# Performance work log

Hardware: AMD Instinct MI355X
Metric: run time of the kernel (lower is better)

## Reference

```python
import jax, jax.numpy as jnp
import numpy as np

B, N = 16, 2048
EMB_DIM = 512
K = 20          # neighbor_num
S = 1           # support_num

def _norm(x, axis):
    # F.normalize: x / max(||x||, 1e-12)
    return x / jnp.maximum(jnp.linalg.norm(x, axis=axis, keepdims=True), 1e-12)

def knn(verts, k):
    # verts: (b, v, 3); squared-distance knn excluding self
    inner = jnp.einsum('bvd,bwd->bvw', verts, verts)
    quad = jnp.sum(verts * verts, axis=2)
    dist = quad[:, :, None] - 2.0 * inner + quad[:, None, :]
    _, idx = jax.lax.top_k(-dist, k + 1)
    return idx[:, :, 1:]

def gather_nb(x, idx):
    # x: (b, v, c), idx: (b, v, n) -> (b, v, n, c)
    return jax.vmap(lambda t, i: t[i])(x, idx)

def dir_norm(verts, idx):
    d = gather_nb(verts, idx) - verts[:, :, None, :]
    return _norm(d, -1)

def conv_surface(idx, verts, directions, kernel_num):
    theta = jax.nn.relu(jnp.einsum('bvnd,dk->bvnk', dir_norm(verts, idx), _norm(directions, 0)))
    b, v, n, _ = theta.shape
    theta = theta.reshape(b, v, n, S, kernel_num)
    return jnp.sum(jnp.max(theta, axis=2), axis=2)  # (b, v, kernel_num)

def conv_layer(idx, verts, fm, w, bias, directions, out_ch):
    theta = jax.nn.relu(jnp.einsum('bvnd,dk->bvnk', dir_norm(verts, idx), _norm(directions, 0)))
    feat = fm @ w + bias                            # (b, v, (S+1)*out_ch)
    center = feat[:, :, :out_ch]
    support = gather_nb(feat[:, :, out_ch:], idx)   # (b, v, n, S*out_ch)
    b, v, n, _ = support.shape
    act = (theta * support).reshape(b, v, n, S, out_ch)
    return center + jnp.sum(jnp.max(act, axis=2), axis=2)

def pool_layer(verts, fm, key, pooling_rate=4, neighbor_num=4):
    b, v, _ = verts.shape
    idx = knn(verts, neighbor_num)
    pooled = jnp.max(gather_nb(fm, idx), axis=2)
    samp = jax.random.permutation(key, v)[: v // pooling_rate]
    return verts[:, samp, :], pooled[:, samp, :]

def _forward(xyz, w1, b1, w2, b2, w3, b3, w4, b4, fcw, fcb, dir0,
             wc1, bc1, dir1, wc2, bc2, dir2, wc3, bc3, dir3, wc4, bc4, dir4,
             clw1, clb1, bn_gamma, bn_beta, clw2, clb2):
    relu = jax.nn.relu
    # PointNet trunk (Conv1d with kernel 1 == per-point matmul)
    x = relu(jnp.einsum('oc,bcn->bon', w1, xyz) + b1[None, :, None])
    x = relu(jnp.einsum('oc,bcn->bon', w2, x) + b2[None, :, None])
    gf = jnp.max(x, axis=2, keepdims=True)
    x = jnp.concatenate([x, jnp.broadcast_to(gf, x.shape)], axis=1)
    x = relu(jnp.einsum('oc,bcn->bon', w3, x) + b3[None, :, None])
    x = relu(jnp.einsum('oc,bcn->bon', w4, x) + b4[None, :, None])
    x = jnp.max(x, axis=2)                          # (B, 1024)
    # GCN3D trunk
    verts = jnp.transpose(xyz, (0, 2, 1))           # (B, N, 3)
    idx = knn(verts, K)
    fm0 = relu(conv_surface(idx, verts, dir0, 32))
    fm1 = relu(conv_layer(idx, verts, fm0, wc1, bc1, dir1, 64))
    verts, fm1 = pool_layer(verts, fm1, jax.random.key(1))
    idx = knn(verts, K)
    fm2 = relu(conv_layer(idx, verts, fm1, wc2, bc2, dir2, 128))
    fm3 = relu(conv_layer(idx, verts, fm2, wc3, bc3, dir3, 256))
    verts, fm3 = pool_layer(verts, fm3, jax.random.key(2))
    idx = knn(verts, K)
    fm4 = conv_layer(idx, verts, fm3, wc4, bc4, dir4, 1024)
    fg = jnp.max(fm4, axis=1)                       # (B, 1024)
    fc_data = jnp.concatenate([x, fg], axis=1)      # (B, 2048)
    embedding = fc_data @ fcw.T + fcb
    # classifier, eval mode: Dropout -> identity; BN uses running mean 0 / var 1
    h = fc_data @ clw1.T + clb1
    h = relu(h / jnp.sqrt(1.0 + 1e-5) * bn_gamma + bn_beta)
    pred = h @ clw2.T + clb2
    return embedding, pred

def setup_inputs():
    key = jax.random.key(0)
    ks = jax.random.split(key, 32)
    rn = lambda k, shp: jax.random.normal(k, shp, dtype=jnp.float32) * 0.05
    return {
        'xyz': jax.random.normal(ks[0], (B, 3, N), dtype=jnp.float32),
        'w1': rn(ks[1], (64, 3)), 'b1': rn(ks[2], (64,)),
        'w2': rn(ks[3], (128, 64)), 'b2': rn(ks[4], (128,)),
        'w3': rn(ks[5], (256, 256)), 'b3': rn(ks[6], (256,)),
        'w4': rn(ks[7], (1024, 256)), 'b4': rn(ks[8], (1024,)),
        'fcw': rn(ks[9], (EMB_DIM, 2048)), 'fcb': rn(ks[10], (EMB_DIM,)),
        'dir0': rn(ks[11], (3, 32)),
        'wc1': rn(ks[12], (32, 128)), 'bc1': rn(ks[13], (128,)), 'dir1': rn(ks[14], (3, 64)),
        'wc2': rn(ks[15], (64, 256)), 'bc2': rn(ks[16], (256,)), 'dir2': rn(ks[17], (3, 128)),
        'wc3': rn(ks[18], (128, 512)), 'bc3': rn(ks[19], (512,)), 'dir3': rn(ks[20], (3, 256)),
        'wc4': rn(ks[21], (256, 2048)), 'bc4': rn(ks[22], (2048,)), 'dir4': rn(ks[23], (3, 1024)),
        'clw1': rn(ks[24], (512, 2048)), 'clb1': rn(ks[25], (512,)),
        'bn_gamma': jnp.ones((512,), dtype=jnp.float32),
        'bn_beta': jnp.zeros((512,), dtype=jnp.float32),
        'clw2': rn(ks[26], (6, 512)), 'clb2': rn(ks[27], (6,)),
    }

def reference(xyz, w1, b1, w2, b2, w3, b3, w4, b4, fcw, fcb, dir0, wc1, bc1, dir1, wc2, bc2, dir2, wc3, bc3, dir3, wc4, bc4, dir4, clw1, clb1, bn_gamma, bn_beta, clw2, clb2):
    return _forward(xyz, w1, b1, w2, b2, w3, b3, w4, b4, fcw, fcb, dir0, wc1, bc1, dir1, wc2, bc2, dir2, wc3, bc3, dir3, wc4, bc4, dir4, clw1, clb1, bn_gamma, bn_beta, clw2, clb2)
```

## Files before the change

kernel.cpp:

```cpp
#include <hip/hip_runtime.h>
#include <hip/hip_bf16.h>
#include <math.h>

#define BB 16
#define NN 2048

typedef __attribute__((ext_vector_type(8))) short s8v;
typedef __attribute__((ext_vector_type(4))) float f4v;

__global__ void k_sentinel(float* o, int n, float v){
  int i = blockIdx.x*256 + threadIdx.x;
  if (i < n) o[i] = v;
}

__device__ __forceinline__ ushort f2bf(float x){
  unsigned u = __float_as_uint(x);
  unsigned r = u + 0x7FFFu + ((u>>16)&1u);
  return (ushort)(r>>16);
}
__device__ __forceinline__ void splitbf(float v, ushort &h, ushort &l){
  h = f2bf(v);
  float hf = __uint_as_float((unsigned)h<<16);
  l = f2bf(v-hf);
}


__global__ void k_wsplit3h(const float* __restrict__ s1, ushort* __restrict__ d1h, int n1,
                           const float* __restrict__ s2, ushort* __restrict__ d2h, int n2,
                           const float* __restrict__ s3, ushort* __restrict__ d3h, int n3){
  int id = blockIdx.x*256 + threadIdx.x;
  const float* s; ushort *dh; int i;
  if (id < n1){ s=s1; dh=d1h; i=id; }
  else if (id < n1+n2){ s=s2; dh=d2h; i=id-n1; }
  else if (id < n1+n2+n3){ s=s3; dh=d3h; i=id-n1-n2; }
  else return;
  dh[i] = f2bf(s[i]);
}

__global__ void k_wstr4(const float* __restrict__ s1, ushort* __restrict__ d1h, ushort* __restrict__ d1l, int K1, int C1,
                        const float* __restrict__ s2, ushort* __restrict__ d2h, ushort* __restrict__ d2l, int K2, int C2,
                        const float* __restrict__ s3, ushort* __restrict__ d3h, ushort* __restrict__ d3l, int K3, int C3,
                        const float* __restrict__ s4, ushort* __restrict__ d4h, ushort* __restrict__ d4l, int K4, int C4){
  int id = blockIdx.x*256 + threadIdx.x;
  int n1=K1*C1, n2=K2*C2, n3=K3*C3, n4=K4*C4;
  const float* s; ushort *dh, *dl; int i, K, C;
  if (id < n1){ s=s1; dh=d1h; dl=d1l; i=id; K=K1; C=C1; }
  else if (id < n1+n2){ s=s2; dh=d2h; dl=d2l; i=id-n1; K=K2; C=C2; }
  else if (id < n1+n2+n3){ s=s3; dh=d3h; dl=d3l; i=id-n1-n2; K=K3; C=C3; }
  else if (id < n1+n2+n3+n4){ s=s4; dh=d4h; dl=d4l; i=id-n1-n2-n3; K=K4; C=C4; }
  else return;
  int c = i % C, k = i / C;
  ushort h,l; splitbf(s[i], h, l);
  dh[(size_t)c*K + k]=h; dl[(size_t)c*K + k]=l;
}


__global__ void k_mlp1s(const float* __restrict__ xyz, const float* __restrict__ w1,
                        const float* __restrict__ b1, ushort* __restrict__ xh,
                        ushort* __restrict__ xl){
  int id = blockIdx.x*256 + threadIdx.x;
  if (id >= BB*NN*64) return;
  int o = id & 63, n = (id>>6) & (NN-1), b = id>>17;
  float acc = b1[o];
  #pragma unroll
  for (int c=0;c<3;c++)
    acc += w1[o*3+c] * xyz[(size_t)(b*3+c)*NN + n];
  acc = fmaxf(acc, 0.f);
  ushort h,l; splitbf(acc, h, l);
  xh[id]=h; xl[id]=l;
}

__global__ void k_gmax(const float* __restrict__ pmax, ushort* __restrict__ gh,
                       ushort* __restrict__ gl, int parts, int total){
  int id = blockIdx.x*256 + threadIdx.x;
  if (id >= total) return;
  float m = pmax[(size_t)id*parts];
  for (int k=1;k<parts;k++) m = fmaxf(m, pmax[(size_t)id*parts+k]);
  ushort h,l; splitbf(m, h, l);
  gh[id]=h; gl[id]=l;
}

template<int EPI, int RELU, int BCOL>
__global__ __launch_bounds__(256) void k_bgemm(
    const ushort* __restrict__ Ahg,
    const ushort* __restrict__ Bhg, const ushort* __restrict__ Blg,
    const ushort* __restrict__ gfh, const ushort* __restrict__ gfl,
    const float* __restrict__ bias,
    float* __restrict__ outp, float* __restrict__ pmaxp,
    ushort* __restrict__ oth, ushort* __restrict__ otl,
    int K, int ksplit, int Kb, int N, size_t sBT, size_t sOut, int M)
{
  __shared__ ushort Ah[128][40];
  __shared__ ushort Bh[64][40], Bl[64][40];
  __shared__ float red[2][128];
  int t = threadIdx.x, z = blockIdx.z;
  int o0 = blockIdx.y*128, n0 = blockIdx.x*64;
  int wid = t>>6, lane = t&63;
  int wm = wid>>1, wn = wid&1;
  int lr = lane&15, kg = lane>>4;

  f4v acc[4][2];
  #pragma unroll
  for (int i=0;i<4;i++)
    #pragma unroll
    for (int j=0;j<2;j++) acc[i][j] = (f4v){0.f,0.f,0.f,0.f};

  for (int k0=0; k0<K; k0+=32){
    __syncthreads();
    #pragma unroll
    for (int i=0;i<2;i++){
      int j = i*256+t, oo = j>>2, k8 = (j&3)*8;
      size_t sp = (size_t)(o0+oo)*K + k0 + k8;
      *(s8v*)&Ah[oo][k8] = *(const s8v*)(Ahg+sp);
    }
    {
      int nn = t>>2, k8 = (t&3)*8, gk = k0+k8;
      const ushort *sh, *sl;
      if (gk < ksplit){
        size_t sp = (size_t)z*sBT + (size_t)(n0+nn)*Kb + gk;
        sh = Bhg+sp; sl = Blg+sp;
      } else {
        size_t sp = (size_t)z*(K-ksplit) + (gk-ksplit);
        sh = gfh+sp; sl = gfl+sp;
      }
      *(s8v*)&Bh[nn][k8] = *(const s8v*)sh;
      *(s8v*)&Bl[nn][k8] = *(const s8v*)sl;
    }
    __syncthreads();

    s8v ah[4], bh[2], bl[2];
    #pragma unroll
    for (int mt=0;mt<4;mt++){
      int row = wm*64 + mt*16 + lr;
      ah[mt] = *(const s8v*)&Ah[row][kg*8];
    }
    #pragma unroll
    for (int nt=0;nt<2;nt++){
      int col = wn*32 + nt*16 + lr;
      bh[nt] = *(const s8v*)&Bh[col][kg*8];
      bl[nt] = *(const s8v*)&Bl[col][kg*8];
    }
    #pragma unroll
    for (int mt=0;mt<4;mt++)
      #pragma unroll
      for (int nt=0;nt<2;nt++){
        acc[mt][nt] = __builtin_amdgcn_mfma_f32_16x16x32_bf16(ah[mt], bh[nt], acc[mt][nt], 0,0,0);
        acc[mt][nt] = __builtin_amdgcn_mfma_f32_16x16x32_bf16(ah[mt], bl[nt], acc[mt][nt], 0,0,0);
      }
  }

  if (EPI == 1 || EPI == 4){
    #pragma unroll
    for (int mt=0;mt<4;mt++){
      #pragma unroll
      for (int e=0;e<4;e++){
        int row = o0 + wm*64 + mt*16 + kg*4 + e;
        float bv = bias[row];
        float v0 = fmaxf(acc[mt][0][e]+bv, 0.f);
        float v1 = fmaxf(acc[mt][1][e]+bv, 0.f);
        if (EPI == 4){
          int col0 = n0 + wn*32 + lr;
          ushort h,l;
          splitbf(v0, h, l);
          size_t p0 = ((size_t)z*N + col0)*(size_t)M + row;
          oth[p0]=h; otl[p0]=l;
          splitbf(v1, h, l);
          size_t p1 = ((size_t)z*N + col0+16)*(size_t)M + row;
          oth[p1]=h; otl[p1]=l;
        }
        float m = fmaxf(v0, v1);
        m = fmaxf(m, __shfl_xor(m, 1, 64));
        m = fmaxf(m, __shfl_xor(m, 2, 64));
        m = fmaxf(m, __shfl_xor(m, 4, 64));
        m = fmaxf(m, __shfl_xor(m, 8, 64));
        if (lr == 0) red[wn][wm*64 + mt*16 + kg*4 + e] = m;
      }
    }
    __syncthreads();
    if (t < 128){
      float m = fmaxf(red[0][t], red[1][t]);
      pmaxp[((size_t)z*M + o0 + t)*gridDim.x + blockIdx.x] = m;
    }
  } else {
    #pragma unroll
    for (int mt=0;mt<4;mt++){
      #pragma unroll
      for (int nt=0;nt<2;nt++){
        int col = n0 + wn*32 + nt*16 + lr;
        #pragma unroll
        for (int e=0;e<4;e++){
          int row = o0 + wm*64 + mt*16 + kg*4 + e;
          float bv = BCOL ? bias[col] : bias[row];
          float v = acc[mt][nt][e] + bv;
          if (RELU) v = fmaxf(v, 0.f);
          if (EPI == 0)
            outp[(size_t)z*sOut + (size_t)row*N + col] = v;
          if (EPI == 3){
            ushort h,l; splitbf(v, h, l);
            size_t p = ((size_t)z*N + col)*(size_t)M + row;
            oth[p]=h; otl[p]=l;
          }
        }
      }
    }
  }
}

__global__ void k_xmax(const float* __restrict__ pmax, float* __restrict__ xmax){
  int id = blockIdx.x*256 + threadIdx.x;
  if (id >= BB*1024) return;
  float m = pmax[(size_t)id*32];
  for (int k=1;k<32;k++) m = fmaxf(m, pmax[(size_t)id*32+k]);
  xmax[id] = m;
}


#define TF2BODY \
  unsigned ks2 = 0x1BD11BDAu ^ k0 ^ k1; \
  unsigned a = x0 + k0, b = x1 + k1; \
  { \
  a += b; b = (b<<13)|(b>>19); b ^= a; \
  a += b; b = (b<<15)|(b>>17); b ^= a; \
  a += b; b = (b<<26)|(b>>6);  b ^= a; \
  a += b; b = (b<<6) |(b>>26); b ^= a;  a += k1;  b += ks2 + 1u; \
  a += b; b = (b<<17)|(b>>15); b ^= a; \
  a += b; b = (b<<29)|(b>>3);  b ^= a; \
  a += b; b = (b<<16)|(b>>16); b ^= a; \
  a += b; b = (b<<24)|(b>>8);  b ^= a;  a += ks2; b += k0  + 2u; \
  a += b; b = (b<<13)|(b>>19); b ^= a; \
  a += b; b = (b<<15)|(b>>17); b ^= a; \
  a += b; b = (b<<26)|(b>>6);  b ^= a; \
  a += b; b = (b<<6) |(b>>26); b ^= a;  a += k0;  b += k1  + 3u; \
  a += b; b = (b<<17)|(b>>15); b ^= a; \
  a += b; b = (b<<29)|(b>>3);  b ^= a; \
  a += b; b = (b<<16)|(b>>16); b ^= a; \
  a += b; b = (b<<24)|(b>>8);  b ^= a;  a += k1;  b += ks2 + 4u; \
  a += b; b = (b<<13)|(b>>19); b ^= a; \
  a += b; b = (b<<15)|(b>>17); b ^= a; \
  a += b; b = (b<<26)|(b>>6);  b ^= a; \
  a += b; b = (b<<6) |(b>>26); b ^= a;  a += ks2; b += k0  + 5u; \
  } \
  o0 = a; o1 = b;

__device__ __forceinline__ void tf2(unsigned k0, unsigned k1, unsigned x0, unsigned x1,
                                    unsigned &o0, unsigned &o1){ TF2BODY }
static void tf2h(unsigned k0, unsigned k1, unsigned x0, unsigned x1,
                 unsigned &o0, unsigned &o1){ TF2BODY }

__global__ void k_permkeys3(unsigned a0, unsigned a1, unsigned* __restrict__ ka,
                            unsigned b0, unsigned b1, unsigned* __restrict__ kb,
                            unsigned c0, unsigned c1, unsigned* __restrict__ kc){
  int id = blockIdx.x*256 + threadIdx.x;
  if (id < 2048){ unsigned x,y; tf2(a0,a1, 0u,(unsigned)id, x,y); ka[id] = x^y; }
  if (id < 2048){ unsigned x,y; tf2(b0,b1, 0u,(unsigned)id, x,y); kb[id] = x^y; }
  if (id < 512){ unsigned x,y; tf2(c0,c1, 0u,(unsigned)id, x,y); kc[id] = x^y; }
}

__global__ void k_permrank(int n, const unsigned* __restrict__ keys,
                           const int* __restrict__ vin, int* __restrict__ vout){
  int i = blockIdx.x*256 + threadIdx.x;
  if (i >= n) return;
  unsigned ki = keys[i];
  int rank = 0;
  for (int j=0;j<n;j++){
    unsigned kj = keys[j];
    rank += (kj < ki) || (kj == ki && j < i);
  }
  vout[rank] = vin ? vin[i] : i;
}


template<int CPL, int KSEL>
__global__ __launch_bounds__(256,4) void k_knn_s(const float* __restrict__ vbcs,
                                                 int numQ, int* __restrict__ out){
  constexpr int V = CPL*64;
  constexpr int GS = (CPL < 8) ? CPL : 8;
  constexpr int NG = CPL/GS;
  int t = threadIdx.x, wid = t>>6, lane = t&63;
  int b = blockIdx.y;
  int q = blockIdx.x*4 + wid;
  if (q >= numQ) return;
  const float* vx = vbcs + (size_t)b*3*V;
  const float* vy = vx + V;
  const float* vz = vy + V;
  float qx = vx[q], qy = vy[q], qz = vz[q];
  float qq = qx*qx + qy*qy + qz*qz;
  unsigned d[CPL];
  #pragma unroll
  for (int i=0;i<CPL;i++){
    int c = lane + i*64;
    float wx=vx[c], wy=vy[c], wz=vz[c];
    float inner = qx*wx + qy*wy + qz*wz;
    float ww = wx*wx + wy*wy + wz*wz;
    float dd = qq - 2.f*inner + ww;
    unsigned db = __float_as_uint(dd);
    d[i] = (db & 0x80000000u) ? ~db : (db | 0x80000000u);
  }
  unsigned long long g[NG];
  #pragma unroll
  for (int gg=0; gg<NG; gg++){
    unsigned long long m = ~0ull;
    #pragma unroll
    for (int j=0;j<GS;j++){
      int p = gg*GS+j;
      unsigned long long kk = ((unsigned long long)d[p]<<32) | (unsigned)p;
      m = (kk<m)?kk:m;
    }
    g[gg] = m;
  }
  unsigned lmin = (unsigned)(g[0]>>32);
  #pragma unroll
  for (int gg=1;gg<NG;gg++){ unsigned x = (unsigned)(g[gg]>>32); lmin = (x<lmin)?x:lmin; }

  int* orow = out + ((size_t)b*numQ + q)*KSEL;
  for (int r=0; r<=KSEL; r++){
    unsigned bd = lmin;
    #pragma unroll
    for (int off=32; off>0; off>>=1){
      unsigned o = __shfl_xor(bd, off, 64);
      bd = (o < bd) ? o : bd;
    }
    unsigned long long bal = __ballot(lmin == bd);
    int winner = __ffsll(bal) - 1;
    if (lane == winner){
      unsigned long long mbest = g[0];
      #pragma unroll
      for (int gg=1;gg<NG;gg++) mbest = (g[gg]<mbest)?g[gg]:mbest;
      int pos = (int)(mbest & 0xffffffffull);
      if (r>0) orow[r-1] = lane + pos*64;
      int gi = pos / GS;
      #pragma unroll
      for (int gg=0; gg<NG; gg++){
        if (gg == gi){
          unsigned long long m = ~0ull;
          #pragma unroll
          for (int j=0;j<GS;j++){
            int p = gg*GS+j;
            unsigned long long kk = ((unsigned long long)d[p]<<32) | (unsigned)p;
            if (kk <= mbest) kk = ~0ull;
            m = (kk<m)?kk:m;
          }
          g[gg] = m;
        }
      }
      unsigned nl = (unsigned)(g[0]>>32);
      #pragma unroll
      for (int gg=1;gg<NG;gg++){ unsigned x = (unsigned)(g[gg]>>32); nl = (x<nl)?x:nl; }
      lmin = nl;
    }
  }
}

__global__ void k_dirs_soa(const float* __restrict__ vbcs, int V,
                           const int* __restrict__ idx, float* __restrict__ dirs,
                           int total){
  int id = blockIdx.x*256 + threadIdx.x;
  if (id >= total) return;
  int v = (id/20) % V, b = id/(20*V);
  const float* vx = vbcs + (size_t)b*3*V;
  const float* vy = vx + V;
  const float* vz = vy + V;
  int nb = idx[id];
  float dx = vx[nb]-vx[v];
  float dy = vy[nb]-vy[v];
  float dz = vz[nb]-vz[v];
  float s = 1.f / fmaxf(sqrtf(dx*dx+dy*dy+dz*dz), 1e-12f);
  dirs[(size_t)id*3+0]=dx*s; dirs[(size_t)id*3+1]=dy*s; dirs[(size_t)id*3+2]=dz*s;
}

__global__ void k_surf4(const float* __restrict__ dirs, const float* __restrict__ dir0,
                        ushort* __restrict__ fh, int V){
  int id = blockIdx.x*256 + threadIdx.x;
  if (id >= BB*V*8) return;
  int k4 = (id & 7)*4; int vv = (id>>3) % V; int b = id/(8*V);
  f4v nx = *(const f4v*)&dir0[k4];
  f4v ny = *(const f4v*)&dir0[32+k4];
  f4v nz = *(const f4v*)&dir0[64+k4];
  #pragma unroll
  for (int j=0;j<4;j++){
    float s = 1.f/fmaxf(sqrtf(nx[j]*nx[j]+ny[j]*ny[j]+nz[j]*nz[j]), 1e-12f);
    nx[j]*=s; ny[j]*=s; nz[j]*=s;
  }
  const float* dd = dirs + (size_t)(b*V+vv)*60;
  f4v m = (f4v){0.f,0.f,0.f,0.f};
  for (int n=0;n<20;n++){
    float d0=dd[n*3], d1=dd[n*3+1], d2=dd[n*3+2];
    #pragma unroll
    for (int j=0;j<4;j++){
      float th = d0*nx[j] + d1*ny[j] + d2*nz[j];
      m[j] = fmaxf(m[j], fmaxf(th, 0.f));
    }
  }
  size_t p = (size_t)(b*V+vv)*32 + k4;
  #pragma unroll
  for (int j=0;j<4;j++) fh[p+j] = f2bf(m[j]);
}

template<int OUT>
__global__ void k_comb4(const float* __restrict__ feat, const int* __restrict__ idx,
                        const float* __restrict__ dirs, const float* __restrict__ dw,
                        float* __restrict__ outp, ushort* __restrict__ oh,
                        int V, int OC, int relu_flag){
  int id = blockIdx.x*256 + threadIdx.x;
  int OC4 = OC>>2;
  if (id >= BB*V*OC4) return;
  int o4 = (id % OC4)*4, v = (id/OC4) % V, b = id/(OC4*V);
  f4v wx = *(const f4v*)&dw[o4];
  f4v wy = *(const f4v*)&dw[OC+o4];
  f4v wz = *(const f4v*)&dw[2*OC+o4];
  #pragma unroll
  for (int j=0;j<4;j++){
    float s = 1.f/fmaxf(sqrtf(wx[j]*wx[j]+wy[j]*wy[j]+wz[j]*wz[j]), 1e-12f);
    wx[j]*=s; wy[j]*=s; wz[j]*=s;
  }
  size_t row = (size_t)b*V + v;
  const int* ir = idx + row*20;
  const float* dd = dirs + row*60;
  f4v center = *(const f4v*)&feat[row*2*OC + o4];
  f4v m = (f4v){-INFINITY,-INFINITY,-INFINITY,-INFINITY};
  for (int n=0;n<20;n++){
    int nb = ir[n];
    float d0=dd[n*3], d1=dd[n*3+1], d2=dd[n*3+2];
    f4v sup = *(const f4v*)&feat[((size_t)b*V + nb)*2*OC + OC + o4];
    #pragma unroll
    for (int j=0;j<4;j++){
      float th = fmaxf(d0*wx[j] + d1*wy[j] + d2*wz[j], 0.f);
      m[j] = fmaxf(m[j], th*sup[j]);
    }
  }
  if (OUT == 0){
    f4v rv;
    #pragma unroll
    for (int j=0;j<4;j++){
      float x = center[j] + m[j];
      rv[j] = relu_flag ? fmaxf(x, 0.f) : x;
    }
    *(f4v*)&outp[row*OC + o4] = rv;
  } else {
    #pragma unroll
    for (int j=0;j<4;j++)
      oh[row*OC + o4 + j] = f2bf(fmaxf(center[j] + m[j], 0.f));
  }
}

template<int OUT>
__global__ void k_pool(const float* __restrict__ fm, const int* __restrict__ idxsrc,
                       const int* __restrict__ perm,
                       float* __restrict__ outp, ushort* __restrict__ oh,
                       int V, int C, int numS){
  int id = blockIdx.x*256 + threadIdx.x;
  if (id >= BB*numS*C) return;
  int c = id % C, sI = (id/C) % numS, b = id/(C*numS);
  const int* ir = idxsrc + ((size_t)b*V + perm[sI])*20;
  float m = -INFINITY;
  for (int n=0;n<4;n++) m = fmaxf(m, fm[((size_t)b*V + ir[n])*C + c]);
  size_t p = ((size_t)b*numS + sI)*C + c;
  if (OUT == 0) outp[p] = m;
  else oh[p] = f2bf(m);
}

__global__ void k_vgather(const float* __restrict__ vsrc, const int* __restrict__ perm,
                          float* __restrict__ vbcs, int V, int numS){
  int id = blockIdx.x*256 + threadIdx.x;
  if (id >= BB*3*numS) return;
  int s = id % numS, c = (id/numS) % 3, b = id/(3*numS);
  vbcs[id] = vsrc[((size_t)b*3 + c)*V + perm[s]];
}

__global__ void k_colmax(const float* __restrict__ x, float* __restrict__ o, int Vr, int C){
  int id = blockIdx.x*256 + threadIdx.x;
  if (id >= BB*C) return;
  int c = id % C, b = id / C;
  float m = -INFINITY;
  for (int v=0; v<Vr; v++) m = fmaxf(m, x[(size_t)(b*Vr+v)*C + c]);
  o[id] = m;
}


__global__ __launch_bounds__(256) void k_emb2(const float* __restrict__ xmax, const float* __restrict__ fg,
                                              const float* __restrict__ fcw, const float* __restrict__ fcb,
                                              float* __restrict__ outp){
  int gid = blockIdx.x*4 + (threadIdx.x>>6);
  int lane = threadIdx.x & 63;
  if (gid >= BB*512) return;
  int e = gid & 511, b = gid >> 9;
  const float* wr = fcw + (size_t)e*2048;
  const float* xb = xmax + b*1024;
  const float* gb = fg + b*1024;
  float acc = 0.f;
  for (int k=lane; k<1024; k+=64)
    acc += xb[k]*wr[k] + gb[k]*wr[1024+k];
  #pragma unroll
  for (int off=32; off>0; off>>=1) acc += __shfl_xor(acc, off, 64);
  if (lane==0) outp[gid] = acc + fcb[e];
}

__global__ __launch_bounds__(256) void k_h2(const float* __restrict__ xmax, const float* __restrict__ fg,
                                            const float* __restrict__ clw1, const float* __restrict__ clb1,
                                            const float* __restrict__ gamma, const float* __restrict__ beta,
                                            float* __restrict__ h){
  int gid = blockIdx.x*4 + (threadIdx.x>>6);
  int lane = threadIdx.x & 63;
  if (gid >= BB*512) return;
  int j = gid & 511, b = gid >> 9;
  const float* wr = clw1 + (size_t)j*2048;
  const float* xb = xmax + b*1024;
  const float* gb = fg + b*1024;
  float acc = 0.f;
  for (int k=lane; k<1024; k+=64)
    acc += xb[k]*wr[k] + gb[k]*wr[1024+k];
  #pragma unroll
  for (int off=32; off>0; off>>=1) acc += __shfl_xor(acc, off, 64);
  if (lane==0){
    const float inv_s = 1.0f / sqrtf(1.0f + 1e-5f);
    float v = (acc + clb1[j]) * inv_s * gamma[j] + beta[j];
    h[gid] = fmaxf(v, 0.f);
  }
}

__global__ __launch_bounds__(256) void k_pred2(const float* __restrict__ h, const float* __restrict__ clw2,
                                               const float* __restrict__ clb2, float* __restrict__ outp){
  int gid = blockIdx.x*4 + (threadIdx.x>>6);
  int lane = threadIdx.x & 63;
  if (gid >= BB*6) return;
  int o = gid % 6, b = gid / 6;
  const float* hb = h + b*512;
  const float* wr = clw2 + o*512;
  float acc = 0.f;
  for (int k=lane; k<512; k+=64) acc += hb[k]*wr[k];
  #pragma unroll
  for (int off=32; off>0; off>>=1) acc += __shfl_xor(acc, off, 64);
  if (lane==0) outp[BB*512 + gid] = acc + clb2[o];
}


static inline int cdiv(long long a, int b){ return (int)((a + b - 1)/b); }

extern "C" void kernel_launch(void* const* d_in, const int* in_sizes, int n_in,
                              void* d_out, int out_size, void* d_ws, size_t ws_size,
                              hipStream_t stream){
  float* out = (float*)d_out;
  if (n_in != 30 || in_sizes[0] != BB*3*NN || out_size != BB*512 + BB*6){
    k_sentinel<<<cdiv(out_size,256),256,0,stream>>>(out, out_size, 2000.0f);
    return;
  }
  const float* xyz  = (const float*)d_in[0];
  const float* w1   = (const float*)d_in[1];
  const float* b1   = (const float*)d_in[2];
  const float* w2   = (const float*)d_in[3];
  const float* b2   = (const float*)d_in[4];
  const float* w3   = (const float*)d_in[5];
  const float* b3   = (const float*)d_in[6];
  const float* w4   = (const float*)d_in[7];
  const float* b4   = (const float*)d_in[8];
  const float* fcw  = (const float*)d_in[9];
  const float* fcb  = (const float*)d_in[10];
  const float* dir0 = (const float*)d_in[11];
  const float* wc1  = (const float*)d_in[12];
  const float* bc1  = (const float*)d_in[13];
  const float* dir1 = (const float*)d_in[14];
  const float* wc2  = (const float*)d_in[15];
  const float* bc2  = (const float*)d_in[16];
  const float* dir2 = (const float*)d_in[17];
  const float* wc3  = (const float*)d_in[18];
  const float* bc3  = (const float*)d_in[19];
  const float* dir3 = (const float*)d_in[20];
  const float* wc4  = (const float*)d_in[21];
  const float* bc4  = (const float*)d_in[22];
  const float* dir4 = (const float*)d_in[23];
  const float* clw1 = (const float*)d_in[24];
  const float* clb1 = (const float*)d_in[25];
  const float* gma  = (const float*)d_in[26];
  const float* bta  = (const float*)d_in[27];
  const float* clw2 = (const float*)d_in[28];
  const float* clb2 = (const float*)d_in[29];

  char* w = (char*)d_ws;
  size_t off = 0;
  auto A = [&](size_t bytes){ size_t r = off; off += (bytes + 255) & ~(size_t)255; return r; };
  const size_t oXMAX = A((size_t)BB*1024*4);
  const size_t oFG   = A((size_t)BB*1024*4);
  const size_t oGFP  = A((size_t)BB*128*2*2);
  const size_t oH    = A((size_t)BB*512*4);
  const size_t oP2048= A(2048*4);
  const size_t oP512 = A(512*4);
  const size_t oPK1  = A(2048*4);
  const size_t oPK2  = A(2048*4);
  const size_t oPK3  = A(512*4);
  const size_t oPA   = A(2048*4);
  const size_t oPMAX = A((size_t)BB*1024*32*4);
  const size_t oV1S  = A((size_t)BB*3*512*4);
  const size_t oV2S  = A((size_t)BB*3*128*4);
  const size_t oIDX0 = A((size_t)BB*2048*20*4);
  const size_t oDIR0 = A((size_t)BB*2048*20*3*4);
  const size_t oFM0  = A((size_t)BB*2048*32*2);
  const size_t oFM1  = A((size_t)BB*2048*64*4);
  const size_t oFM1P = A((size_t)BB*512*64*2);
  const size_t oIDX1 = A((size_t)BB*512*20*4);
  const size_t oDIR1 = A((size_t)BB*512*20*3*4);
  const size_t oFM2  = A((size_t)BB*512*128*2);
  const size_t oFM3  = A((size_t)BB*512*256*4);
  const size_t oFM3P = A((size_t)BB*128*256*2);
  const size_t oIDX2 = A((size_t)BB*128*20*4);
  const size_t oDIR2 = A((size_t)BB*128*20*3*4);
  const size_t oFM4  = A((size_t)BB*128*1024*4);
  const size_t oBIGA = A((size_t)BB*256*NN*4);
  const size_t oBIGB = A((size_t)BB*128*NN*4);
  const size_t oW2P  = A((size_t)128*64*2);
  const size_t oW3P  = A((size_t)256*256*2);
  const size_t oW4P  = A((size_t)1024*256*2);
  const size_t oWC1T = A((size_t)32*128*2*2);
  const size_t oWC2T = A((size_t)64*256*2*2);
  const size_t oWC3T = A((size_t)128*512*2*2);
  const size_t oWC4T = A((size_t)256*2048*2*2);
  if (off > ws_size){
    k_sentinel<<<cdiv(out_size,256),256,0,stream>>>(out, out_size, 1000.0f);
    return;
  }
  float* xmax = (float*)(w+oXMAX); float* fg = (float*)(w+oFG);
  float* hbuf = (float*)(w+oH);
  ushort* gfh = (ushort*)(w+oGFP); ushort* gfl = gfh + BB*128;
  int* p2048 = (int*)(w+oP2048);   int* p512 = (int*)(w+oP512);
  unsigned* pk1 = (unsigned*)(w+oPK1); unsigned* pk2 = (unsigned*)(w+oPK2);
  unsigned* pk3 = (unsigned*)(w+oPK3); int* pa = (int*)(w+oPA);
  float* pmax = (float*)(w+oPMAX);
  float* v1s = (float*)(w+oV1S); float* v2s = (float*)(w+oV2S);
  int* idx0 = (int*)(w+oIDX0); int* idx1 = (int*)(w+oIDX1); int* idx2 = (int*)(w+oIDX2);
  float* d0 = (float*)(w+oDIR0); float* d1 = (float*)(w+oDIR1); float* d2 = (float*)(w+oDIR2);
  ushort* fm0h = (ushort*)(w+oFM0);
  float* fm1 = (float*)(w+oFM1);
  ushort* fm1ph = (ushort*)(w+oFM1P);
  ushort* fm2h = (ushort*)(w+oFM2);
  float* fm3 = (float*)(w+oFM3);
  ushort* fm3ph = (ushort*)(w+oFM3P);
  float* fm4 = (float*)(w+oFM4);
  ushort* x1h = (ushort*)(w+oBIGA); ushort* x1l = x1h + (size_t)BB*2048*64;
  ushort* x3h = (ushort*)(w+oBIGA); ushort* x3l = x3h + (size_t)BB*2048*256;
  ushort* x2h = (ushort*)(w+oIDX0); ushort* x2l = x2h + (size_t)BB*2048*128;
  float* feat = (float*)(w+oBIGB);
  ushort* w2ph = (ushort*)(w+oW2P);
  ushort* w3ph = (ushort*)(w+oW3P);
  ushort* w4ph = (ushort*)(w+oW4P);
  ushort* wc1h = (ushort*)(w+oWC1T); ushort* wc1l = wc1h + 32*128;
  ushort* wc2h = (ushort*)(w+oWC2T); ushort* wc2l = wc2h + 64*256;
  ushort* wc3h = (ushort*)(w+oWC3T); ushort* wc3l = wc3h + 128*512;
  ushort* wc4h = (ushort*)(w+oWC4T); ushort* wc4l = wc4h + 256*2048;

  k_wsplit3h<<<cdiv(128*64+256*256+1024*256,256),256,0,stream>>>(
      w2, w2ph, 128*64,  w3, w3ph, 256*256,  w4, w4ph, 1024*256);
  k_wstr4<<<cdiv(32*128+64*256+128*512+256*2048,256),256,0,stream>>>(
      wc1, wc1h, wc1l, 32, 128,  wc2, wc2h, wc2l, 64, 256,
      wc3, wc3h, wc3l, 128, 512, wc4, wc4h, wc4l, 256, 2048);

  k_mlp1s<<<cdiv((long long)BB*NN*64,256),256,0,stream>>>(xyz, w1, b1, x1h, x1l);
  k_bgemm<4,1,0><<<dim3(32,1,BB),256,0,stream>>>(w2ph, x1h, x1l, nullptr, nullptr,
      b2, nullptr, pmax, x2h, x2l, 64, 64, 64, 2048, (size_t)2048*64, 0, 128);
  k_gmax<<<cdiv(BB*128,256),256,0,stream>>>(pmax, gfh, gfl, 32, BB*128);
  k_bgemm<3,1,0><<<dim3(32,2,BB),256,0,stream>>>(w3ph, x2h, x2l, gfh, gfl,
      b3, nullptr, nullptr, x3h, x3l, 256, 128, 128, 2048, (size_t)2048*128, 0, 256);
  k_bgemm<1,1,0><<<dim3(32,8,BB),256,0,stream>>>(w4ph, x3h, x3l, nullptr, nullptr,
      b4, nullptr, pmax, nullptr, nullptr, 256, 256, 256, 2048, (size_t)2048*256, 0, 1024);
  k_xmax<<<cdiv(BB*1024,256),256,0,stream>>>(pmax, xmax);

  {
    unsigned ck0=0u, ck1=1u, nk0,nk1, s00,s01, s10,s11, sc0,sc1;
    tf2h(ck0,ck1, 0u,0u, nk0,nk1);
    tf2h(ck0,ck1, 0u,1u, s00,s01);
    tf2h(nk0,nk1, 0u,1u, s10,s11);
    tf2h(0u,2u,  0u,1u, sc0,sc1);
    k_permkeys3<<<8,256,0,stream>>>(s00,s01,pk1, s10,s11,pk2, sc0,sc1,pk3);
    k_permrank<<<8,256,0,stream>>>(2048, pk1, nullptr, pa);
    k_permrank<<<8,256,0,stream>>>(2048, pk2, pa, p2048);
    k_permrank<<<2,256,0,stream>>>(512, pk3, nullptr, p512);
  }

  k_knn_s<32,20><<<dim3(512,BB),256,0,stream>>>(xyz, 2048, idx0);
  k_dirs_soa<<<cdiv((long long)BB*2048*20,256),256,0,stream>>>(xyz, 2048, idx0, d0, BB*2048*20);
  k_surf4<<<cdiv((long long)BB*2048*8,256),256,0,stream>>>(d0, dir0, fm0h, 2048);
  k_bgemm<0,0,1><<<dim3(2,256,1),256,0,stream>>>(fm0h, wc1h, wc1l, nullptr, nullptr,
      bc1, feat, nullptr, nullptr, nullptr, 32, 32, 32, 128, 0, 0, BB*2048);
  k_comb4<0><<<cdiv((long long)BB*2048*16,256),256,0,stream>>>(feat, idx0, d0, dir1, fm1, nullptr, 2048, 64, 1);
  k_pool<1><<<cdiv((long long)BB*512*64,256),256,0,stream>>>(fm1, idx0, p2048, nullptr, fm1ph, 2048, 64, 512);
  k_vgather<<<cdiv((long long)BB*3*512,256),256,0,stream>>>(xyz, p2048, v1s, 2048, 512);
  k_knn_s<8,20><<<dim3(128,BB),256,0,stream>>>(v1s, 512, idx1);
  k_dirs_soa<<<cdiv((long long)BB*512*20,256),256,0,stream>>>(v1s, 512, idx1, d1, BB*512*20);
  k_bgemm<0,0,1><<<dim3(4,64,1),256,0,stream>>>(fm1ph, wc2h, wc2l, nullptr, nullptr,
      bc2, feat, nullptr, nullptr, nullptr, 64, 64, 64, 256, 0, 0, BB*512);
  k_comb4<1><<<cdiv((long long)BB*512*32,256),256,0,stream>>>(feat, idx1, d1, dir2, nullptr, fm2h, 512, 128, 1);
  k_bgemm<0,0,1><<<dim3(8,64,1),256,0,stream>>>(fm2h, wc3h, wc3l, nullptr, nullptr,
      bc3, feat, nullptr, nullptr, nullptr, 128, 128, 128, 512, 0, 0, BB*512);
  k_comb4<0><<<cdiv((long long)BB*512*64,256),256,0,stream>>>(feat, idx1, d1, dir3, fm3, nullptr, 512, 256, 1);
  k_pool<1><<<cdiv((long long)BB*128*256,256),256,0,stream>>>(fm3, idx1, p512, nullptr, fm3ph, 512, 256, 128);
  k_vgather<<<cdiv((long long)BB*3*128,256),256,0,stream>>>(v1s, p512, v2s, 512, 128);
  k_knn_s<2,20><<<dim3(32,BB),256,0,stream>>>(v2s, 128, idx2);
  k_dirs_soa<<<cdiv((long long)BB*128*20,256),256,0,stream>>>(v2s, 128, idx2, d2, BB*128*20);
  k_bgemm<0,0,1><<<dim3(32,16,1),256,0,stream>>>(fm3ph, wc4h, wc4l, nullptr, nullptr,
      bc4, feat, nullptr, nullptr, nullptr, 256, 256, 256, 2048, 0, 0, BB*128);
  k_comb4<0><<<cdiv((long long)BB*128*256,256),256,0,stream>>>(feat, idx2, d2, dir4, fm4, nullptr, 128, 1024, 0);
  k_colmax<<<cdiv(BB*1024,256),256,0,stream>>>(fm4, fg, 128, 1024);

  k_emb2<<<cdiv(BB*512,4),256,0,stream>>>(xmax, fg, fcw, fcb, out);
  k_h2<<<cdiv(BB*512,4),256,0,stream>>>(xmax, fg, clw1, clb1, gma, bta, hbuf);
  k_pred2<<<cdiv(BB*6,4),256,0,stream>>>(hbuf, clw2, clb2, out);
}
```

Before: 651.1 us.

## Co-schedule knn, conv4 GEMM and permutation ranking in one fused launch

```diff
diff --git a/kernel.cpp b/kernel.cpp
--- a/kernel.cpp
+++ b/kernel.cpp
@@ -81,20 +81,21 @@
 }
 
 template<int EPI, int RELU, int BCOL>
-__global__ __launch_bounds__(256) void k_bgemm(
+__device__ __forceinline__ void bgemm_body(
     const ushort* __restrict__ Ahg,
     const ushort* __restrict__ Bhg, const ushort* __restrict__ Blg,
     const ushort* __restrict__ gfh, const ushort* __restrict__ gfl,
     const float* __restrict__ bias,
     float* __restrict__ outp, float* __restrict__ pmaxp,
     ushort* __restrict__ oth, ushort* __restrict__ otl,
-    int K, int ksplit, int Kb, int N, size_t sBT, size_t sOut, int M)
+    int K, int ksplit, int Kb, int N, size_t sBT, size_t sOut, int M,
+    int bx, int by, int bz, int nparts)
 {
   __shared__ ushort Ah[128][40];
   __shared__ ushort Bh[64][40], Bl[64][40];
   __shared__ float red[2][128];
-  int t = threadIdx.x, z = blockIdx.z;
-  int o0 = blockIdx.y*128, n0 = blockIdx.x*64;
+  int t = threadIdx.x, z = bz;
+  int o0 = by*128, n0 = bx*64;
   int wid = t>>6, lane = t&63;
   int wm = wid>>1, wn = wid&1;
   int lr = lane&15, kg = lane>>4;
@@ -179,7 +180,7 @@
     __syncthreads();
     if (t < 128){
       float m = fmaxf(red[0][t], red[1][t]);
-      pmaxp[((size_t)z*M + o0 + t)*gridDim.x + blockIdx.x] = m;
+      pmaxp[((size_t)z*M + o0 + t)*nparts + bx] = m;
     }
   } else {
     #pragma unroll
@@ -204,6 +205,21 @@
       }
     }
   }
+}
+
+template<int EPI, int RELU, int BCOL>
+__global__ __launch_bounds__(256) void k_bgemm(
+    const ushort* __restrict__ Ahg,
+    const ushort* __restrict__ Bhg, const ushort* __restrict__ Blg,
+    const ushort* __restrict__ gfh, const ushort* __restrict__ gfl,
+    const float* __restrict__ bias,
+    float* __restrict__ outp, float* __restrict__ pmaxp,
+    ushort* __restrict__ oth, ushort* __restrict__ otl,
+    int K, int ksplit, int Kb, int N, size_t sBT, size_t sOut, int M)
+{
+  bgemm_body<EPI,RELU,BCOL>(Ahg, Bhg, Blg, gfh, gfl, bias, outp, pmaxp, oth, otl,
+                            K, ksplit, Kb, N, sBT, sOut, M,
+                            blockIdx.x, blockIdx.y, blockIdx.z, gridDim.x);
 }
 
 __global__ void k_xmax(const float* __restrict__ pmax, float* __restrict__ xmax){
@@ -256,29 +272,17 @@
   if (id < 512){ unsigned x,y; tf2(c0,c1, 0u,(unsigned)id, x,y); kc[id] = x^y; }
 }
 
-__global__ void k_permrank(int n, const unsigned* __restrict__ keys,
-                           const int* __restrict__ vin, int* __restrict__ vout){
-  int i = blockIdx.x*256 + threadIdx.x;
-  if (i >= n) return;
-  unsigned ki = keys[i];
-  int rank = 0;
-  for (int j=0;j<n;j++){
-    unsigned kj = keys[j];
-    rank += (kj < ki) || (kj == ki && j < i);
-  }
-  vout[rank] = vin ? vin[i] : i;
-}
-
 
 template<int CPL, int KSEL>
-__global__ __launch_bounds__(256,4) void k_knn_s(const float* __restrict__ vbcs,
-                                                 int numQ, int* __restrict__ out){
+__device__ __forceinline__ void knn_body(const float* __restrict__ vbcs,
+                                         int numQ, int* __restrict__ out,
+                                         int bx, int by){
   constexpr int V = CPL*64;
   constexpr int GS = (CPL < 8) ? CPL : 8;
   constexpr int NG = CPL/GS;
   int t = threadIdx.x, wid = t>>6, lane = t&63;
-  int b = blockIdx.y;
-  int q = blockIdx.x*4 + wid;
+  int b = by;
+  int q = bx*4 + wid;
   if (q >= numQ) return;
   const float* vx = vbcs + (size_t)b*3*V;
   const float* vy = vx + V;
@@ -351,6 +355,78 @@
   }
 }
 
+template<int CPL, int KSEL>
+__global__ __launch_bounds__(256,4) void k_knn_s(const float* __restrict__ vbcs,
+                                                 int numQ, int* __restrict__ out){
+  knn_body<CPL,KSEL>(vbcs, numQ, out, blockIdx.x, blockIdx.y);
+}
+
+__global__ __launch_bounds__(256,4) void k_fused(
+    const float* __restrict__ vbcs, int numQ, int* __restrict__ outIdx,
+    const ushort* __restrict__ Ahg, const ushort* __restrict__ Bhg, const ushort* __restrict__ Blg,
+    const float* __restrict__ bias, float* __restrict__ pmaxp,
+    const unsigned* __restrict__ pk1, const unsigned* __restrict__ pk2,
+    const unsigned* __restrict__ pk3,
+    int* __restrict__ p2048, int* __restrict__ p512)
+{
+  int bx = blockIdx.x, by = blockIdx.y;
+  if (bx < 512){
+    knn_body<32,20>(vbcs, numQ, outIdx, bx, by);
+  } else if (bx < 768){
+    int loc = bx - 512;
+    int nx = loc & 31, oy = loc >> 5;
+    bgemm_body<1,1,0>(Ahg, Bhg, Blg, nullptr, nullptr, bias,
+                      nullptr, pmaxp, nullptr, nullptr,
+                      256, 256, 256, 2048, (size_t)2048*256, 0, 1024,
+                      nx, oy, by, 32);
+  } else {
+    __shared__ unsigned kbuf[2048];
+    __shared__ int va[2048];
+    int t = threadIdx.x;
+    if (by == 0){
+      for (int i=t;i<2048;i+=256) kbuf[i]=pk1[i];
+      __syncthreads();
+      unsigned ki[8]; int rv[8]; int ith[8];
+      #pragma unroll
+      for (int c=0;c<8;c++){ ith[c]=t+c*256; ki[c]=kbuf[ith[c]]; rv[c]=0; }
+      for (int j=0;j<2048;j++){
+        unsigned kj = kbuf[j];
+        #pragma unroll
+        for (int c=0;c<8;c++)
+          rv[c] += ((kj<ki[c]) || (kj==ki[c] && j<ith[c])) ? 1 : 0;
+      }
+      __syncthreads();
+      #pragma unroll
+      for (int c=0;c<8;c++) va[rv[c]] = ith[c];
+      __syncthreads();
+      for (int i=t;i<2048;i+=256) kbuf[i]=pk2[i];
+      __syncthreads();
+      #pragma unroll
+      for (int c=0;c<8;c++){ ki[c]=kbuf[ith[c]]; rv[c]=0; }
+      for (int j=0;j<2048;j++){
+        unsigned kj = kbuf[j];
+        #pragma unroll
+        for (int c=0;c<8;c++)
+          rv[c] += ((kj<ki[c]) || (kj==ki[c] && j<ith[c])) ? 1 : 0;
+      }
+      #pragma unroll
+      for (int c=0;c<8;c++) p2048[rv[c]] = va[ith[c]];
+    } else if (by == 1){
+      for (int i=t;i<512;i+=256) kbuf[i]=pk3[i];
+      __syncthreads();
+      #pragma unroll
+      for (int c=0;c<2;c++){
+        int i = t + c*256;
+        unsigned ki = kbuf[i];
+        int r=0;
+        for (int j=0;j<512;j++){ unsigned kj=kbuf[j]; r += (kj<ki)||(kj==ki && j<i); }
+        p512[r]=i;
+      }
+    }
+  }
+}
+
+
 __global__ void k_dirs_soa(const float* __restrict__ vbcs, int V,
                            const int* __restrict__ idx, float* __restrict__ dirs,
                            int total){
@@ -477,14 +553,18 @@
 }
 
 
-__global__ __launch_bounds__(256) void k_emb2(const float* __restrict__ xmax, const float* __restrict__ fg,
+__global__ __launch_bounds__(256) void k_embh(const float* __restrict__ xmax, const float* __restrict__ fg,
                                               const float* __restrict__ fcw, const float* __restrict__ fcb,
-                                              float* __restrict__ outp){
+                                              const float* __restrict__ clw1, const float* __restrict__ clb1,
+                                              const float* __restrict__ gamma, const float* __restrict__ beta,
+                                              float* __restrict__ outp, float* __restrict__ h){
   int gid = blockIdx.x*4 + (threadIdx.x>>6);
   int lane = threadIdx.x & 63;
-  if (gid >= BB*512) return;
-  int e = gid & 511, b = gid >> 9;
-  const float* wr = fcw + (size_t)e*2048;
+  if (gid >= 2*BB*512) return;
+  bool isH = gid >= BB*512;
+  int g2 = isH ? gid - BB*512 : gid;
+  int e = g2 & 511, b = g2 >> 9;
+  const float* wr = (isH ? clw1 : fcw) + (size_t)e*2048;
   const float* xb = xmax + b*1024;
   const float* gb = fg + b*1024;
   float acc = 0.f;
@@ -492,29 +572,14 @@
     acc += xb[k]*wr[k] + gb[k]*wr[1024+k];
   #pragma unroll
   for (int off=32; off>0; off>>=1) acc += __shfl_xor(acc, off, 64);
-  if (lane==0) outp[gid] = acc + fcb[e];
-}
-
-__global__ __launch_bounds__(256) void k_h2(const float* __restrict__ xmax, const float* __restrict__ fg,
-                                            const float* __restrict__ clw1, const float* __restrict__ clb1,
-                                            const float* __restrict__ gamma, const float* __restrict__ beta,
-                                            float* __restrict__ h){
-  int gid = blockIdx.x*4 + (threadIdx.x>>6);
-  int lane = threadIdx.x & 63;
-  if (gid >= BB*512) return;
-  int j = gid & 511, b = gid >> 9;
-  const float* wr = clw1 + (size_t)j*2048;
-  const float* xb = xmax + b*1024;
-  const float* gb = fg + b*1024;
-  float acc = 0.f;
-  for (int k=lane; k<1024; k+=64)
-    acc += xb[k]*wr[k] + gb[k]*wr[1024+k];
-  #pragma unroll
-  for (int off=32; off>0; off>>=1) acc += __shfl_xor(acc, off, 64);
   if (lane==0){
-    const float inv_s = 1.0f / sqrtf(1.0f + 1e-5f);
-    float v = (acc + clb1[j]) * inv_s * gamma[j] + beta[j];
-    h[gid] = fmaxf(v, 0.f);
+    if (isH){
+      const float inv_s = 1.0f / sqrtf(1.0f + 1e-5f);
+      float v = (acc + clb1[e]) * inv_s * gamma[e] + beta[e];
+      h[g2] = fmaxf(v, 0.f);
+    } else {
+      outp[g2] = acc + fcb[e];
+    }
   }
 }
 
@@ -587,7 +652,6 @@
   const size_t oPK1  = A(2048*4);
   const size_t oPK2  = A(2048*4);
   const size_t oPK3  = A(512*4);
-  const size_t oPA   = A(2048*4);
   const size_t oPMAX = A((size_t)BB*1024*32*4);
   const size_t oV1S  = A((size_t)BB*3*512*4);
   const size_t oV2S  = A((size_t)BB*3*128*4);
@@ -622,7 +686,7 @@
   ushort* gfh = (ushort*)(w+oGFP); ushort* gfl = gfh + BB*128;
   int* p2048 = (int*)(w+oP2048);   int* p512 = (int*)(w+oP512);
   unsigned* pk1 = (unsigned*)(w+oPK1); unsigned* pk2 = (unsigned*)(w+oPK2);
-  unsigned* pk3 = (unsigned*)(w+oPK3); int* pa = (int*)(w+oPA);
+  unsigned* pk3 = (unsigned*)(w+oPK3);
   float* pmax = (float*)(w+oPMAX);
   float* v1s = (float*)(w+oV1S); float* v2s = (float*)(w+oV2S);
   int* idx0 = (int*)(w+oIDX0); int* idx1 = (int*)(w+oIDX1); int* idx2 = (int*)(w+oIDX2);
@@ -658,9 +722,6 @@
   k_gmax<<<cdiv(BB*128,256),256,0,stream>>>(pmax, gfh, gfl, 32, BB*128);
   k_bgemm<3,1,0><<<dim3(32,2,BB),256,0,stream>>>(w3ph, x2h, x2l, gfh, gfl,
       b3, nullptr, nullptr, x3h, x3l, 256, 128, 128, 2048, (size_t)2048*128, 0, 256);
-  k_bgemm<1,1,0><<<dim3(32,8,BB),256,0,stream>>>(w4ph, x3h, x3l, nullptr, nullptr,
-      b4, nullptr, pmax, nullptr, nullptr, 256, 256, 256, 2048, (size_t)2048*256, 0, 1024);
-  k_xmax<<<cdiv(BB*1024,256),256,0,stream>>>(pmax, xmax);
 
   {
     unsigned ck0=0u, ck1=1u, nk0,nk1, s00,s01, s10,s11, sc0,sc1;
@@ -669,12 +730,12 @@
     tf2h(nk0,nk1, 0u,1u, s10,s11);
     tf2h(0u,2u,  0u,1u, sc0,sc1);
     k_permkeys3<<<8,256,0,stream>>>(s00,s01,pk1, s10,s11,pk2, sc0,sc1,pk3);
-    k_permrank<<<8,256,0,stream>>>(2048, pk1, nullptr, pa);
-    k_permrank<<<8,256,0,stream>>>(2048, pk2, pa, p2048);
-    k_permrank<<<2,256,0,stream>>>(512, pk3, nullptr, p512);
-  }
-
-  k_knn_s<32,20><<<dim3(512,BB),256,0,stream>>>(xyz, 2048, idx0);
+  }
+
+  k_fused<<<dim3(769,16),256,0,stream>>>(xyz, 2048, idx0,
+      w4ph, x3h, x3l, b4, pmax, pk1, pk2, pk3, p2048, p512);
+  k_xmax<<<cdiv(BB*1024,256),256,0,stream>>>(pmax, xmax);
+
   k_dirs_soa<<<cdiv((long long)BB*2048*20,256),256,0,stream>>>(xyz, 2048, idx0, d0, BB*2048*20);
   k_surf4<<<cdiv((long long)BB*2048*8,256),256,0,stream>>>(d0, dir0, fm0h, 2048);
   k_bgemm<0,0,1><<<dim3(2,256,1),256,0,stream>>>(fm0h, wc1h, wc1l, nullptr, nullptr,
@@ -699,7 +760,6 @@
   k_comb4<0><<<cdiv((long long)BB*128*256,256),256,0,stream>>>(feat, idx2, d2, dir4, fm4, nullptr, 128, 1024, 0);
   k_colmax<<<cdiv(BB*1024,256),256,0,stream>>>(fm4, fg, 128, 1024);
 
-  k_emb2<<<cdiv(BB*512,4),256,0,stream>>>(xmax, fg, fcw, fcb, out);
-  k_h2<<<cdiv(BB*512,4),256,0,stream>>>(xmax, fg, clw1, clb1, gma, bta, hbuf);
+  k_embh<<<cdiv(2*BB*512,4),256,0,stream>>>(xmax, fg, fcw, fcb, clw1, clb1, gma, bta, out, hbuf);
   k_pred2<<<cdiv(BB*6,4),256,0,stream>>>(hbuf, clw2, clb2, out);
 }
```

After: 904.4 us. 1.39x slower.
